# Optimization experiments

Measured on AMD Instinct MI355X. Metric: run time of the kernel, lower is better.

## Reference

```python
import jax, jax.numpy as jnp
import numpy as np


def setup_inputs() -> dict:
    key = jax.random.key(0)
    k1, k2, k3, k4, k5 = jax.random.split(key, 5)
    B, L, G, DG = 2, 8192, 256, 8
    D = G * DG
    x1 = jax.random.normal(k1, (B, L, G, DG), dtype=jnp.float32)
    x2 = jax.random.normal(k2, (B, L, G, DG), dtype=jnp.float32)
    v = jax.random.normal(k3, (B, L, G, DG), dtype=jnp.float32)
    # implicit/explicit filter output: one length-L kernel per group, scaled down
    # like a decaying long-conv filter so outputs stay O(1)
    t = jnp.arange(L, dtype=jnp.float32)
    decay = jnp.exp(-t / 1024.0)[None, :]  # (1, L)
    h = jax.random.normal(k4, (G, L), dtype=jnp.float32) * decay / jnp.sqrt(jnp.float32(L))
    conv_bias = jax.random.normal(k5, (D,), dtype=jnp.float32)
    return {"x1": x1, "x2": x2, "v": v, "h": h, "conv_bias": conv_bias}


def reference(x1, x2, v, h, conv_bias):
    # x1, x2, v: (B, L, G, DG); h: (G, L); conv_bias: (G*DG,)
    B, L, G, DG = x1.shape
    D = G * DG
    # 'b l g dg -> b (g dg) l'
    x1c = x1.reshape(B, L, D).transpose(0, 2, 1)  # (B, D, L)
    x2c = x2.reshape(B, L, D).transpose(0, 2, 1)
    vc = v.reshape(B, L, D).transpose(0, 2, 1)

    kv = x2c * vc  # pre-gate: (B, D, L)

    fft_size = 2 * L  # causal (linear) convolution via zero-padded FFT
    # each group's filter is shared across its DG channels
    h_rep = jnp.repeat(h, DG, axis=0)  # (D, L)
    kv_f = jnp.fft.rfft(kv.astype(jnp.float32), n=fft_size)
    h_f = jnp.fft.rfft(h_rep.astype(jnp.float32), n=fft_size)
    y = jnp.fft.irfft(kv_f * h_f[None], n=fft_size)[..., :L]  # (B, D, L)

    y = y + kv * conv_bias[None, :, None]  # skip/bias term
    z = x1c * y  # post-gate (identity gating activation)

    # back to (B, L, D)
    return z.transpose(0, 2, 1)
```

## Files before the change

kernel.cpp:

```cpp
#include <hip/hip_runtime.h>
#include <hip/hip_bf16.h>

typedef __attribute__((ext_vector_type(8))) __bf16 bf16x8;
typedef __attribute__((ext_vector_type(4))) __bf16 bf16x4;
typedef __attribute__((ext_vector_type(4))) float  f32x4;

#define L_LEN   8192
#define D_DIM   2048
#define G_NUM   256
#define HP      8320
#define HS      680
#define KVS     136

__global__ __launch_bounds__(256) void prep_kv_kernel(
    const float* __restrict__ x2, const float* __restrict__ v,
    __bf16* __restrict__ kvout)
{
  __shared__ __bf16 sT[64 * 66];
  const int tid = threadIdx.x;
  const int l0 = blockIdx.x << 6;
  const int d0 = blockIdx.y << 6;
  const int b  = blockIdx.z;
  const int col = tid & 63, r4 = tid >> 6;
#pragma unroll
  for (int rr = 0; rr < 16; ++rr) {
    const int lloc = (rr << 2) + r4;
    const size_t idx = ((size_t)(b * L_LEN + l0 + lloc)) * D_DIM + d0 + col;
    sT[col * 66 + lloc] = (__bf16)(x2[idx] * v[idx]);
  }
  __syncthreads();
  const int ch = tid >> 2, seg = tid & 3;
  const int gch = d0 + ch;
  const int row = ((gch >> 3) << 4) + (b << 3) + (gch & 7);
  bf16x8 a0, a1;
#pragma unroll
  for (int k = 0; k < 8; ++k) {
    a0[k] = sT[ch * 66 + (seg << 4) + k];
    a1[k] = sT[ch * 66 + (seg << 4) + 8 + k];
  }
  __bf16* dst = kvout + (size_t)row * L_LEN + l0 + (seg << 4);
  *(bf16x8*)dst = a0;
  *(bf16x8*)(dst + 8) = a1;
}

__global__ __launch_bounds__(256) void prep_h_kernel(
    const float* __restrict__ h, __bf16* __restrict__ hr)
{
  const unsigned i = blockIdx.x * 256u + threadIdx.x;
  const unsigned g = i / (8u * HP);
  const unsigned r = i - g * (8u * HP);
  const unsigned s = r / HP;
  const unsigned z = r - s * HP;
  const int P = 8255 - (int)z - (int)s;
  __bf16 val = (__bf16)0.0f;
  if (P >= 0 && P < 8192) val = (__bf16)h[(size_t)g * 8192 + P];
  hr[i] = val;
}

__global__ __launch_bounds__(256, 4) void conv_kernel(
    const __bf16* __restrict__ KV, const __bf16* __restrict__ HR,
    const float* __restrict__ x1, const float* __restrict__ bias,
    float* __restrict__ out)
{
  __shared__ __bf16 sKV[16 * KVS];
  __shared__ __bf16 sH[8 * HS];

  const int g   = blockIdx.x;
  const int jb  = 15 - (int)blockIdx.y;
  const int l0  = jb << 9;
  const int tid = threadIdx.x;
  const int lane = tid & 63, wv = tid >> 6;
  const int m = lane & 15, q = lane >> 4;

  const __bf16* __restrict__ KVg = KV + (size_t)g * (16 * L_LEN);
  const __bf16* __restrict__ HRg = HR + (size_t)g * (8 * HP);

  f32x4 acc0 = {0.f,0.f,0.f,0.f}, acc1 = acc0, acc2 = acc0, acc3 = acc0,
        acc4 = acc0, acc5 = acc0, acc6 = acc0, acc7 = acc0;

  bf16x8 zed;
#pragma unroll
  for (int k = 0; k < 8; ++k) zed[k] = (__bf16)0.0f;

  const int cst = tid >> 4, tst = (tid & 15) << 3;
  const int s_c   = (7 - m) & 7;
  const int bbase = m * KVS + (q << 3);

  const int send = l0 + 512;
  for (int tb = 0; tb < send; tb += 128) {
    __syncthreads();
    *(bf16x8*)&sKV[cst * KVS + tst] = *(const bf16x8*)&KVg[cst * L_LEN + tb + tst];
    const int Bv = 8255 - l0 + tb;
    const int Y0 = (Bv - 518) & ~7;
    for (int u = tid; u < 8 * 82; u += 256) {
      const int s   = u / 82;
      const int off = (u - s * 82) << 3;
      const int yy  = Y0 + off;
      bf16x8 w = zed;
      if (yy + 8 <= HP) w = *(const bf16x8*)&HRg[s * HP + yy];
      *(bf16x8*)&sH[s * HS + off] = w;
    }
    __syncthreads();

    const int zbase = Bv - (wv << 7) - m + (q << 3);
    const int abase = s_c * HS + (zbase - s_c - Y0) - 112;
    const int thr   = l0 + (wv << 7) + 16 - tb;

#define CONV_STEP(i, accv)                                                      \
    if ((jj << 5) < thr + ((i) << 4)) {                                         \
      const bf16x8 afr =                                                        \
          *(const bf16x8*)&sH[abase + ((7 + (jj << 1) - (i)) << 4)];            \
      accv = __builtin_amdgcn_mfma_f32_16x16x32_bf16(afr, bfrag, accv, 0, 0, 0);\
    }

#pragma unroll
    for (int jj = 0; jj < 4; ++jj) {
      const bf16x8 bfrag = *(const bf16x8*)&sKV[bbase + (jj << 5)];
      CONV_STEP(0, acc0)
      CONV_STEP(1, acc1)
      CONV_STEP(2, acc2)
      CONV_STEP(3, acc3)
      CONV_STEP(4, acc4)
      CONV_STEP(5, acc5)
      CONV_STEP(6, acc6)
      CONV_STEP(7, acc7)
    }
#undef CONV_STEP
  }

  const int c = m;
  const int bb = c >> 3, dg = c & 7;
  const float bv = bias[(g << 3) + dg];

#define CONV_EPI(i, accv) {                                                     \
    const int l = l0 + (wv << 7) + ((i) << 4) + (q << 2);                       \
    const bf16x4 kv4 = *(const bf16x4*)&KVg[c * L_LEN + l];                     \
    for (int r = 0; r < 4; ++r) {                                               \
      const float y = accv[r] + (float)kv4[r] * bv;                             \
      const size_t oidx = ((size_t)(bb * L_LEN + l + r)) * D_DIM + (g << 3) + dg;\
      out[oidx] = x1[oidx] * y;                                                 \
    } }

  CONV_EPI(0, acc0)
  CONV_EPI(1, acc1)
  CONV_EPI(2, acc2)
  CONV_EPI(3, acc3)
  CONV_EPI(4, acc4)
  CONV_EPI(5, acc5)
  CONV_EPI(6, acc6)
  CONV_EPI(7, acc7)
#undef CONV_EPI
}

extern "C" void kernel_launch(void* const* d_in, const int* in_sizes, int n_in,
                              void* d_out, int out_size, void* d_ws, size_t ws_size,
                              hipStream_t stream)
{
  const float* x1 = (const float*)d_in[0];
  const float* x2 = (const float*)d_in[1];
  const float* v  = (const float*)d_in[2];
  const float* h  = (const float*)d_in[3];
  const float* cb = (const float*)d_in[4];
  float* out = (float*)d_out;

  __bf16* kv = (__bf16*)d_ws;
  __bf16* hr = kv + (size_t)G_NUM * 16 * L_LEN;

  prep_kv_kernel<<<dim3(L_LEN / 64, D_DIM / 64, 2), 256, 0, stream>>>(x2, v, kv);
  prep_h_kernel<<<(G_NUM * 8 * HP) / 256, 256, 0, stream>>>(h, hr);
  conv_kernel<<<dim3(G_NUM, 16), 256, 0, stream>>>(kv, hr, x1, cb, out);
}
```

Baseline: 834.3 us.

## Double conv K-tile to 256, reuse sliding A fragments in registers, drop prep smem transpose

The conv kernel now stages 256 time steps of kv and a wider Toeplitz filter window per iteration, which halves the number of barrier-separated loop trips. Inside the tile the eight Toeplitz A fragments are held in registers and shifted by two per B fragment, so each new step loads only two A fragments instead of eight. The per-MFMA causal predicate is replaced by a whole-wave skip once the tile passes the wave's end, so edge tiles do full MFMAs and rely on zero padding for correctness. prep_kv drops its shared-memory transpose and reads strided columns directly, which trades coalesced loads for fewer barriers.

```diff
diff --git a/kernel.cpp b/kernel.cpp
--- a/kernel.cpp
+++ b/kernel.cpp
@@ -9,36 +9,31 @@
 #define D_DIM   2048
 #define G_NUM   256
 #define HP      8320
-#define HS      680
-#define KVS     136
+#define HS      808
+#define KVS     264
 
 __global__ __launch_bounds__(256) void prep_kv_kernel(
     const float* __restrict__ x2, const float* __restrict__ v,
     __bf16* __restrict__ kvout)
 {
-  __shared__ __bf16 sT[64 * 66];
   const int tid = threadIdx.x;
   const int l0 = blockIdx.x << 6;
   const int d0 = blockIdx.y << 6;
   const int b  = blockIdx.z;
-  const int col = tid & 63, r4 = tid >> 6;
-#pragma unroll
-  for (int rr = 0; rr < 16; ++rr) {
-    const int lloc = (rr << 2) + r4;
-    const size_t idx = ((size_t)(b * L_LEN + l0 + lloc)) * D_DIM + d0 + col;
-    sT[col * 66 + lloc] = (__bf16)(x2[idx] * v[idx]);
-  }
-  __syncthreads();
-  const int ch = tid >> 2, seg = tid & 3;
-  const int gch = d0 + ch;
+  const int dl = tid & 63;
+  const int lc = tid >> 6;
+  const int gch = d0 + dl;
   const int row = ((gch >> 3) << 4) + (b << 3) + (gch & 7);
+  const size_t ibase = ((size_t)(b * L_LEN + l0 + (lc << 4))) * D_DIM + gch;
   bf16x8 a0, a1;
 #pragma unroll
   for (int k = 0; k < 8; ++k) {
-    a0[k] = sT[ch * 66 + (seg << 4) + k];
-    a1[k] = sT[ch * 66 + (seg << 4) + 8 + k];
+    const size_t i0 = ibase + (size_t)k * D_DIM;
+    const size_t i1 = ibase + (size_t)(k + 8) * D_DIM;
+    a0[k] = (__bf16)(x2[i0] * v[i0]);
+    a1[k] = (__bf16)(x2[i1] * v[i1]);
   }
-  __bf16* dst = kvout + (size_t)row * L_LEN + l0 + (seg << 4);
+  __bf16* dst = kvout + (size_t)row * L_LEN + l0 + (lc << 4);
   *(bf16x8*)dst = a0;
   *(bf16x8*)(dst + 8) = a1;
 }
@@ -85,16 +80,21 @@
   const int cst = tid >> 4, tst = (tid & 15) << 3;
   const int s_c   = (7 - m) & 7;
   const int bbase = m * KVS + (q << 3);
+  const int wend  = l0 + (wv << 7) + 128;
 
   const int send = l0 + 512;
-  for (int tb = 0; tb < send; tb += 128) {
+  for (int tb = 0; tb < send; tb += 256) {
     __syncthreads();
-    *(bf16x8*)&sKV[cst * KVS + tst] = *(const bf16x8*)&KVg[cst * L_LEN + tb + tst];
+    {
+      const __bf16* src = &KVg[cst * L_LEN + tb + tst];
+      *(bf16x8*)&sKV[cst * KVS + tst]       = *(const bf16x8*)src;
+      *(bf16x8*)&sKV[cst * KVS + tst + 128] = *(const bf16x8*)(src + 128);
+    }
     const int Bv = 8255 - l0 + tb;
     const int Y0 = (Bv - 518) & ~7;
-    for (int u = tid; u < 8 * 82; u += 256) {
-      const int s   = u / 82;
-      const int off = (u - s * 82) << 3;
+    for (int u = tid; u < 8 * 98; u += 256) {
+      const int s   = u / 98;
+      const int off = (u - s * 98) << 3;
       const int yy  = Y0 + off;
       bf16x8 w = zed;
       if (yy + 8 <= HP) w = *(const bf16x8*)&HRg[s * HP + yy];
@@ -102,30 +102,35 @@
     }
     __syncthreads();
 
+    if (tb >= wend) continue;
+
     const int zbase = Bv - (wv << 7) - m + (q << 3);
     const int abase = s_c * HS + (zbase - s_c - Y0) - 112;
-    const int thr   = l0 + (wv << 7) + 16 - tb;
 
-#define CONV_STEP(i, accv)                                                      \
-    if ((jj << 5) < thr + ((i) << 4)) {                                         \
-      const bf16x8 afr =                                                        \
-          *(const bf16x8*)&sH[abase + ((7 + (jj << 1) - (i)) << 4)];            \
-      accv = __builtin_amdgcn_mfma_f32_16x16x32_bf16(afr, bfrag, accv, 0, 0, 0);\
-    }
-
-#pragma unroll
-    for (int jj = 0; jj < 4; ++jj) {
-      const bf16x8 bfrag = *(const bf16x8*)&sKV[bbase + (jj << 5)];
-      CONV_STEP(0, acc0)
-      CONV_STEP(1, acc1)
-      CONV_STEP(2, acc2)
-      CONV_STEP(3, acc3)
-      CONV_STEP(4, acc4)
-      CONV_STEP(5, acc5)
-      CONV_STEP(6, acc6)
-      CONV_STEP(7, acc7)
-    }
-#undef CONV_STEP
+#define AFR(f) (*(const bf16x8*)&sH[abase + ((f) << 4)])
+#define BFR(j) (*(const bf16x8*)&sKV[bbase + ((j) << 5)])
+#define MF(ac, ar) ac = __builtin_amdgcn_mfma_f32_16x16x32_bf16(ar, bq, ac, 0, 0, 0)
+    bf16x8 a0=AFR(0),a1=AFR(1),a2=AFR(2),a3=AFR(3),a4=AFR(4),a5=AFR(5),a6=AFR(6),a7=AFR(7);
+    bf16x8 bq;
+    bq = BFR(0);
+    MF(acc0,a7); MF(acc1,a6); MF(acc2,a5); MF(acc3,a4); MF(acc4,a3); MF(acc5,a2); MF(acc6,a1); MF(acc7,a0);
+    a0 = AFR(8);  a1 = AFR(9);  bq = BFR(1);
+    MF(acc0,a1); MF(acc1,a0); MF(acc2,a7); MF(acc3,a6); MF(acc4,a5); MF(acc5,a4); MF(acc6,a3); MF(acc7,a2);
+    a2 = AFR(10); a3 = AFR(11); bq = BFR(2);
+    MF(acc0,a3); MF(acc1,a2); MF(acc2,a1); MF(acc3,a0); MF(acc4,a7); MF(acc5,a6); MF(acc6,a5); MF(acc7,a4);
+    a4 = AFR(12); a5 = AFR(13); bq = BFR(3);
+    MF(acc0,a5); MF(acc1,a4); MF(acc2,a3); MF(acc3,a2); MF(acc4,a1); MF(acc5,a0); MF(acc6,a7); MF(acc7,a6);
+    a6 = AFR(14); a7 = AFR(15); bq = BFR(4);
+    MF(acc0,a7); MF(acc1,a6); MF(acc2,a5); MF(acc3,a4); MF(acc4,a3); MF(acc5,a2); MF(acc6,a1); MF(acc7,a0);
+    a0 = AFR(16); a1 = AFR(17); bq = BFR(5);
+    MF(acc0,a1); MF(acc1,a0); MF(acc2,a7); MF(acc3,a6); MF(acc4,a5); MF(acc5,a4); MF(acc6,a3); MF(acc7,a2);
+    a2 = AFR(18); a3 = AFR(19); bq = BFR(6);
+    MF(acc0,a3); MF(acc1,a2); MF(acc2,a1); MF(acc3,a0); MF(acc4,a7); MF(acc5,a6); MF(acc6,a5); MF(acc7,a4);
+    a4 = AFR(20); a5 = AFR(21); bq = BFR(7);
+    MF(acc0,a5); MF(acc1,a4); MF(acc2,a3); MF(acc3,a2); MF(acc4,a1); MF(acc5,a0); MF(acc6,a7); MF(acc7,a6);
+#undef MF
+#undef BFR
+#undef AFR
   }
 
   const int c = m;
```

New measurement: 720.8 us. -13.6%, faster.
